# Kernel optimization log

Measured on AMD Instinct MI355X. Metric: run time of the kernel, lower is better.

The kernel has to match this reference:

```python
import jax, jax.numpy as jnp
import numpy as np

NLAYERS = 4
HEADS = 4
HEAD_DIM = 64
C = HEADS * HEAD_DIM  # 256
MAX_LEN = 1024


def setup_inputs() -> dict:
    key = jax.random.key(0)
    k1, k2, k3 = jax.random.split(key, 3)
    B, S = 16, 1024
    x = jax.random.normal(k1, (B, C, 1, S), dtype=jnp.float32)
    # length is only used via its static shape[0]; values are irrelevant
    length = jnp.zeros((MAX_LEN,), dtype=jnp.int32)
    # per-layer 1x1 conv weights, std=0.1 as in the torch init (squeeze the 1x1 spatial dims)
    w = jax.random.normal(k2, (NLAYERS, C, C), dtype=jnp.float32) * 0.1
    # persistent kv buffer
    kv = jax.random.normal(k3, (NLAYERS, HEADS, MAX_LEN, HEAD_DIM), dtype=jnp.float32) * 0.1
    return {"x": x, "length": length, "w": w, "kv": kv}


def reference(x, length, w, kv):
    B, _, _, S = x.shape
    L = length.shape[0]  # static slice length into kv buffer
    scale = 1.0 / jnp.sqrt(jnp.asarray(HEAD_DIM, dtype=x.dtype))
    for i in range(NLAYERS):
        # 1x1 conv == channel projection: (B,C,1,S) -> (B,C,1,S)
        x = jnp.einsum('oc,bchs->bohs', w[i], x)
        # view (B,4,64,S) then permute -> query (B,H,S,D)
        q = x.reshape(B, HEADS, HEAD_DIM, S).transpose(0, 1, 3, 2)
        kvi = kv[i, :, :L]  # (H, L, D); broadcasts over batch like the (1,H,L,D) torch slice
        # scaled dot-product attention with k == v == kvi
        scores = jnp.einsum('bhsd,hld->bhsl', q, kvi) * scale
        attn = jax.nn.softmax(scores, axis=-1)
        o = jnp.einsum('bhsl,hld->bhsd', attn, kvi)  # (B,H,S,D)
        # permute back and merge heads -> (B,256,1,S)
        x = o.transpose(0, 1, 3, 2).reshape(B, C, 1, S)
    return x
```

## Files before the change

kernel.cpp:

```cpp
#include <hip/hip_runtime.h>

#define NL   4
#define NH   4
#define HD   64
#define CD   256
#define SQL  1024
#define BB   16

typedef _Float16 half8 __attribute__((ext_vector_type(8)));
typedef _Float16 half4 __attribute__((ext_vector_type(4)));
typedef _Float16 half2v __attribute__((ext_vector_type(2)));
typedef float    f32x4 __attribute__((ext_vector_type(4)));
typedef unsigned short u16x8 __attribute__((ext_vector_type(8)));

static __device__ __forceinline__ float bf2f(unsigned short u) {
    union { unsigned int i; float f; } v; v.i = ((unsigned int)u) << 16; return v.f;
}
static __device__ __forceinline__ unsigned short f2bf(float f) {
    union { float f; unsigned int i; } v; v.f = f;
    unsigned int u = v.i;
    return (unsigned short)((u + 0x7fffu + ((u >> 16) & 1u)) >> 16);
}

static __device__ __forceinline__ int detect_flag(const void* win) {
    const unsigned int* w = (const unsigned int*)win;
    int cnt = 0;
#pragma unroll 1
    for (int i = 0; i < 64; i++) {
        unsigned int lo = w[i] & 0xFFFFu;
        int e = (int)((lo >> 7) & 0xFF);
        cnt += (e >= 96 && e <= 144) ? 1 : 0;
    }
    return cnt >= 48 ? 1 : 0;
}

__global__ __launch_bounds__(256) void prep_all(const void* __restrict__ xin,
                                                const void* __restrict__ win,
                                                const void* __restrict__ kvin,
                                                _Float16* __restrict__ x16,
                                                _Float16* __restrict__ w16,
                                                _Float16* __restrict__ kaF,
                                                _Float16* __restrict__ vtF) {
    __shared__ __align__(16) _Float16 tile[64][72];
    const int bi = blockIdx.x;
    const int t = threadIdx.x;
    const int isbf = detect_flag(win);

    if (bi < 1024) {
        const int st = bi & 15, ct = (bi >> 4) & 3, b = bi >> 6;
        const int r = t >> 2, seg = t & 3;
        const size_t base = ((size_t)(b * CD + ct * 64 + r)) * SQL + st * 64 + seg * 16;
        float v[16];
        if (isbf) {
            const unsigned short* src = (const unsigned short*)xin + base;
            u16x8 u0 = *(const u16x8*)(src);
            u16x8 u1 = *(const u16x8*)(src + 8);
#pragma unroll
            for (int j = 0; j < 8; j++) { v[j] = bf2f(u0[j]); v[8 + j] = bf2f(u1[j]); }
        } else {
            const float* src = (const float*)xin + base;
#pragma unroll
            for (int c = 0; c < 4; c++) {
                f32x4 a = *(const f32x4*)(src + c * 4);
#pragma unroll
                for (int j = 0; j < 4; j++) v[c * 4 + j] = a[j];
            }
        }
#pragma unroll
        for (int j = 0; j < 16; j++) tile[r][seg * 16 + j] = (_Float16)v[j];
        __syncthreads();
        half8 o0, o1;
#pragma unroll
        for (int j = 0; j < 8; j++) { o0[j] = tile[seg * 16 + j][r]; o1[j] = tile[seg * 16 + 8 + j][r]; }
        _Float16* dt = x16 + ((size_t)(b * SQL + st * 64 + r)) * CD + ct * 64 + seg * 16;
        *(half8*)(dt) = o0;
        *(half8*)(dt + 8) = o1;
    } else if (bi < 1280) {
        const int j2 = bi - 1024;
        const int lt = j2 & 15, ih = j2 >> 4;
        const int r = t >> 2, seg = t & 3;
        const size_t base = ((size_t)(ih * SQL + lt * 64 + r)) * HD + seg * 16;
        float v[16];
        if (isbf) {
            const unsigned short* src = (const unsigned short*)kvin + base;
            u16x8 u0 = *(const u16x8*)(src);
            u16x8 u1 = *(const u16x8*)(src + 8);
#pragma unroll
            for (int j = 0; j < 8; j++) { v[j] = bf2f(u0[j]); v[8 + j] = bf2f(u1[j]); }
        } else {
            const float* src = (const float*)kvin + base;
#pragma unroll
            for (int c = 0; c < 4; c++) {
                f32x4 a = *(const f32x4*)(src + c * 4);
#pragma unroll
                for (int j = 0; j < 4; j++) v[c * 4 + j] = a[j];
            }
        }
#pragma unroll
        for (int j = 0; j < 16; j++) tile[r][seg * 16 + j] = (_Float16)v[j];
        __syncthreads();
        const int l = t & 63, l16 = l & 15, q = l >> 4;
        _Float16* kaB = kaF + ((size_t)ih << 16);
        _Float16* vtB = vtF + ((size_t)ih << 16);
#pragma unroll
        for (int it = 0; it < 2; it++) {
            const int c = (t >> 6) + it * 4;
            const int kd = c >> 1, msp = c & 1;
            half8 ok, ov;
#pragma unroll
            for (int j = 0; j < 4; j++) {
                ok[j]     = tile[msp * 32 + l16][kd * 16 + q * 4 + j];
                ok[4 + j] = tile[msp * 32 + 16 + l16][kd * 16 + q * 4 + j];
                ov[j]     = tile[kd * 16 + q * 4 + j][msp * 32 + l16];
                ov[4 + j] = tile[kd * 16 + q * 4 + j][msp * 32 + 16 + l16];
            }
            *(half8*)(kaB + ((lt * 8 + c) << 9) + l * 8) = ok;
            *(half8*)(vtB + ((lt * 8 + c) << 9) + l * 8) = ov;
        }
    } else {
        const int i = (bi - 1280) * 256 + t;
        const size_t base = (size_t)i * 8;
        half8 h;
        if (isbf) {
            u16x8 u = *(const u16x8*)((const unsigned short*)win + base);
#pragma unroll
            for (int j = 0; j < 8; j++) h[j] = (_Float16)bf2f(u[j]);
        } else {
            const float* p = (const float*)win + base;
            f32x4 a0 = *(const f32x4*)(p);
            f32x4 a1 = *(const f32x4*)(p + 4);
#pragma unroll
            for (int j = 0; j < 4; j++) { h[j] = (_Float16)a0[j]; h[4 + j] = (_Float16)a1[j]; }
        }
        *(half8*)(w16 + base) = h;
    }
}

__global__ __launch_bounds__(256, 2) void layer_fused(const _Float16* __restrict__ xg,
                                                      _Float16* __restrict__ xout,
                                                      const _Float16* __restrict__ w16,
                                                      const _Float16* __restrict__ kaF,
                                                      const _Float16* __restrict__ vtF,
                                                      const void* __restrict__ win,
                                                      void* __restrict__ outp,
                                                      int L) {
    const int sb = blockIdx.x;
    const int h  = blockIdx.y;
    const int b  = blockIdx.z;
    const int t  = threadIdx.x;
    const int wv = t >> 6, lane = t & 63, l16 = lane & 15, quad = lane >> 4;
    const int s0 = sb * 128 + wv * 32;

    f32x4 gacc[4][2];
#pragma unroll
    for (int md = 0; md < 4; md++)
#pragma unroll
        for (int nt = 0; nt < 2; nt++)
#pragma unroll
            for (int r = 0; r < 4; r++) gacc[md][nt][r] = 0.0f;
    const _Float16* wb = w16 + ((size_t)L << 16) + ((size_t)(h * 64) << 8);
#pragma unroll
    for (int kk = 0; kk < 8; kk++) {
        half8 bx[2];
#pragma unroll
        for (int nt = 0; nt < 2; nt++)
            bx[nt] = *(const half8*)(xg + ((size_t)((b << 10) + s0 + nt * 16 + l16) << 8) +
                                     kk * 32 + quad * 8);
#pragma unroll
        for (int md = 0; md < 4; md++) {
            half8 aw = *(const half8*)(wb + ((size_t)(md * 16 + l16) << 8) + kk * 32 + quad * 8);
            gacc[md][0] = __builtin_amdgcn_mfma_f32_16x16x32_f16(aw, bx[0], gacc[md][0], 0, 0, 0);
            gacc[md][1] = __builtin_amdgcn_mfma_f32_16x16x32_f16(aw, bx[1], gacc[md][1], 0, 0, 0);
        }
    }
    half4 qh[4][2];
#pragma unroll
    for (int md = 0; md < 4; md++)
#pragma unroll
        for (int nt = 0; nt < 2; nt++)
#pragma unroll
            for (int r = 0; r < 4; r++)
                qh[md][nt][r] = (_Float16)(gacc[md][nt][r] * 0.180336880111120f);

    half4 ones4;
#pragma unroll
    for (int r = 0; r < 4; r++) ones4[r] = (_Float16)1.0f;

    const _Float16* kaB = kaF + ((size_t)(L * NH + h) << 16);
    const _Float16* vtB = vtF + ((size_t)(L * NH + h) << 16);

    f32x4 oacc[4][2];
    f32x4 osum[2];
#pragma unroll
    for (int md = 0; md < 4; md++)
#pragma unroll
        for (int nt = 0; nt < 2; nt++)
#pragma unroll
            for (int r = 0; r < 4; r++) oacc[md][nt][r] = 0.0f;
#pragma unroll
    for (int nt = 0; nt < 2; nt++)
#pragma unroll
        for (int r = 0; r < 4; r++) osum[nt][r] = 0.0f;

    half8 kab[2][8];
    half8 vab[8];
    f32x4 sttC[4][2];

    auto loadK = [&](int lt, int buf) {
#pragma unroll
        for (int c = 0; c < 8; c++)
            kab[buf][c] = *(const half8*)(kaB + (((lt * 8 + c) << 9) + lane * 8));
    };
    auto loadV = [&](int lt) {
#pragma unroll
        for (int c = 0; c < 8; c++)
            vab[c] = *(const half8*)(vtB + (((lt * 8 + c) << 9) + lane * 8));
    };
    auto doQK = [&](int buf) {
#pragma unroll
        for (int ms = 0; ms < 4; ms++)
#pragma unroll
            for (int nt = 0; nt < 2; nt++)
#pragma unroll
                for (int r = 0; r < 4; r++) sttC[ms][nt][r] = 0.0f;
#pragma unroll
        for (int kd = 0; kd < 4; kd++)
#pragma unroll
            for (int msp = 0; msp < 2; msp++) {
                half8 kk8 = kab[buf][kd * 2 + msp];
                half4 lo = __builtin_shufflevector(kk8, kk8, 0, 1, 2, 3);
                half4 hi = __builtin_shufflevector(kk8, kk8, 4, 5, 6, 7);
#pragma unroll
                for (int nt = 0; nt < 2; nt++) {
                    sttC[msp * 2][nt] = __builtin_amdgcn_mfma_f32_16x16x16f16(
                        lo, qh[kd][nt], sttC[msp * 2][nt], 0, 0, 0);
                    sttC[msp * 2 + 1][nt] = __builtin_amdgcn_mfma_f32_16x16x16f16(
                        hi, qh[kd][nt], sttC[msp * 2 + 1][nt], 0, 0, 0);
                }
            }
    };

    loadK(0, 0);
    loadK(1, 1);
    doQK(0);

#pragma unroll 2
    for (int lt = 0; lt < 16; lt++) {
        const int cb = lt & 1, nb = cb ^ 1;
        if (lt < 14) loadK(lt + 2, cb);
        loadV(lt);

        half4 pb[4][2];
#pragma unroll
        for (int ms = 0; ms < 4; ms++)
#pragma unroll
            for (int nt = 0; nt < 2; nt++) {
                float e0 = __builtin_amdgcn_exp2f(sttC[ms][nt][0]);
                float e1 = __builtin_amdgcn_exp2f(sttC[ms][nt][1]);
                float e2 = __builtin_amdgcn_exp2f(sttC[ms][nt][2]);
                float e3 = __builtin_amdgcn_exp2f(sttC[ms][nt][3]);
                half2v p01 = __builtin_bit_cast(half2v, __builtin_amdgcn_cvt_pkrtz(e0, e1));
                half2v p23 = __builtin_bit_cast(half2v, __builtin_amdgcn_cvt_pkrtz(e2, e3));
                pb[ms][nt] = __builtin_shufflevector(p01, p23, 0, 1, 2, 3);
            }

        if (lt < 15) doQK(nb);

#pragma unroll
        for (int ks = 0; ks < 4; ks++) {
#pragma unroll
            for (int nt = 0; nt < 2; nt++)
                osum[nt] = __builtin_amdgcn_mfma_f32_16x16x16f16(
                    ones4, pb[ks][nt], osum[nt], 0, 0, 0);
#pragma unroll
            for (int mdp = 0; mdp < 2; mdp++) {
                half8 vv8 = vab[ks * 2 + mdp];
                half4 lo = __builtin_shufflevector(vv8, vv8, 0, 1, 2, 3);
                half4 hi = __builtin_shufflevector(vv8, vv8, 4, 5, 6, 7);
#pragma unroll
                for (int nt = 0; nt < 2; nt++) {
                    oacc[mdp * 2][nt] = __builtin_amdgcn_mfma_f32_16x16x16f16(
                        lo, pb[ks][nt], oacc[mdp * 2][nt], 0, 0, 0);
                    oacc[mdp * 2 + 1][nt] = __builtin_amdgcn_mfma_f32_16x16x16f16(
                        hi, pb[ks][nt], oacc[mdp * 2 + 1][nt], 0, 0, 0);
                }
            }
        }
    }

    float inv[2];
#pragma unroll
    for (int nt = 0; nt < 2; nt++) inv[nt] = 1.0f / osum[nt][0];

    if (L < NL - 1) {
#pragma unroll
        for (int md = 0; md < 4; md++)
#pragma unroll
            for (int nt = 0; nt < 2; nt++) {
                const int s = s0 + nt * 16 + l16;
                half4 hv;
#pragma unroll
                for (int r = 0; r < 4; r++) hv[r] = (_Float16)(oacc[md][nt][r] * inv[nt]);
                *(half4*)(xout + (((size_t)((b << 10) + s)) << 8) + (h << 6) + md * 16 + quad * 4) = hv;
            }
    } else if (detect_flag(win)) {
#pragma unroll
        for (int md = 0; md < 4; md++)
#pragma unroll
            for (int nt = 0; nt < 2; nt++) {
                const int s = s0 + nt * 16 + l16;
#pragma unroll
                for (int r = 0; r < 4; r++) {
                    const int c = (h << 6) + md * 16 + quad * 4 + r;
                    ((unsigned short*)outp)[(((size_t)(b * CD + c)) << 10) + s] =
                        f2bf(oacc[md][nt][r] * inv[nt]);
                }
            }
    } else {
#pragma unroll
        for (int md = 0; md < 4; md++)
#pragma unroll
            for (int nt = 0; nt < 2; nt++) {
                const int s = s0 + nt * 16 + l16;
#pragma unroll
                for (int r = 0; r < 4; r++) {
                    const int c = (h << 6) + md * 16 + quad * 4 + r;
                    ((float*)outp)[(((size_t)(b * CD + c)) << 10) + s] =
                        oacc[md][nt][r] * inv[nt];
                }
            }
    }
}

extern "C" void kernel_launch(void* const* d_in, const int* in_sizes, int n_in,
                              void* d_out, int out_size, void* d_ws, size_t ws_size,
                              hipStream_t stream) {
    const void* xin = d_in[0];
    const void* win = d_in[2];
    const void* kvin = d_in[3];

    char* ws = (char*)d_ws;
    const size_t MB = 1u << 20;
    _Float16* xa  = (_Float16*)(ws);
    _Float16* xb  = (_Float16*)(ws + 8 * MB);
    _Float16* w16 = (_Float16*)(ws + 16 * MB);
    _Float16* kaF = (_Float16*)(ws + 17 * MB);
    _Float16* vtF = (_Float16*)(ws + 19 * MB);

    prep_all<<<dim3(1024 + 256 + 128), 256, 0, stream>>>(xin, win, kvin, xa, w16, kaF, vtF);

    _Float16* cur = xa;
    _Float16* nxt = xb;
    for (int i = 0; i < NL; i++) {
        layer_fused<<<dim3(SQL / 128, NH, BB), 256, 0, stream>>>(cur, nxt, w16, kaF, vtF,
                                                                 win, d_out, i);
        _Float16* tmp = cur; cur = nxt; nxt = tmp;
    }
}
```

Measured before the change: 249.0 us.

## Split KV range across wave pairs and combine partial attention in shared memory

```diff
diff --git a/kernel.cpp b/kernel.cpp
--- a/kernel.cpp
+++ b/kernel.cpp
@@ -136,7 +136,7 @@
     }
 }
 
-__global__ __launch_bounds__(256, 2) void layer_fused(const _Float16* __restrict__ xg,
+__global__ __launch_bounds__(256, 4) void layer_fused(const _Float16* __restrict__ xg,
                                                       _Float16* __restrict__ xout,
                                                       const _Float16* __restrict__ w16,
                                                       const _Float16* __restrict__ kaF,
@@ -144,12 +144,15 @@
                                                       const void* __restrict__ win,
                                                       void* __restrict__ outp,
                                                       int L) {
+    __shared__ __align__(16) f32x4 comb[2][9][64];
     const int sb = blockIdx.x;
     const int h  = blockIdx.y;
     const int b  = blockIdx.z;
     const int t  = threadIdx.x;
     const int wv = t >> 6, lane = t & 63, l16 = lane & 15, quad = lane >> 4;
-    const int s0 = sb * 128 + wv * 32;
+    const int pair = wv & 1;
+    const int lhalf = wv >> 1;
+    const int s0 = sb * 64 + pair * 32;
 
     f32x4 gacc[4][2];
 #pragma unroll
@@ -188,6 +191,7 @@
 
     const _Float16* kaB = kaF + ((size_t)(L * NH + h) << 16);
     const _Float16* vtB = vtF + ((size_t)(L * NH + h) << 16);
+    const int lt0 = lhalf * 8;
 
     f32x4 oacc[4][2];
     f32x4 osum[2];
@@ -240,15 +244,15 @@
             }
     };
 
-    loadK(0, 0);
-    loadK(1, 1);
+    loadK(lt0, 0);
+    loadK(lt0 + 1, 1);
     doQK(0);
 
 #pragma unroll 2
-    for (int lt = 0; lt < 16; lt++) {
-        const int cb = lt & 1, nb = cb ^ 1;
-        if (lt < 14) loadK(lt + 2, cb);
-        loadV(lt);
+    for (int i = 0; i < 8; i++) {
+        const int cb = i & 1, nb = cb ^ 1;
+        if (i < 6) loadK(lt0 + i + 2, cb);
+        loadV(lt0 + i);
 
         half4 pb[4][2];
 #pragma unroll
@@ -264,7 +268,7 @@
                 pb[ms][nt] = __builtin_shufflevector(p01, p23, 0, 1, 2, 3);
             }
 
-        if (lt < 15) doQK(nb);
+        if (i < 7) doQK(nb);
 
 #pragma unroll
         for (int ks = 0; ks < 4; ks++) {
@@ -288,47 +292,69 @@
         }
     }
 
-    float inv[2];
-#pragma unroll
-    for (int nt = 0; nt < 2; nt++) inv[nt] = 1.0f / osum[nt][0];
-
-    if (L < NL - 1) {
+    if (lhalf == 1) {
 #pragma unroll
         for (int md = 0; md < 4; md++)
 #pragma unroll
+            for (int nt = 0; nt < 2; nt++)
+                comb[pair][md * 2 + nt][lane] = oacc[md][nt];
+        f32x4 ls;
+        ls[0] = osum[0][0]; ls[1] = osum[1][0]; ls[2] = 0.0f; ls[3] = 0.0f;
+        comb[pair][8][lane] = ls;
+    }
+    __syncthreads();
+    if (lhalf == 0) {
+#pragma unroll
+        for (int md = 0; md < 4; md++)
+#pragma unroll
             for (int nt = 0; nt < 2; nt++) {
-                const int s = s0 + nt * 16 + l16;
-                half4 hv;
-#pragma unroll
-                for (int r = 0; r < 4; r++) hv[r] = (_Float16)(oacc[md][nt][r] * inv[nt]);
-                *(half4*)(xout + (((size_t)((b << 10) + s)) << 8) + (h << 6) + md * 16 + quad * 4) = hv;
-            }
-    } else if (detect_flag(win)) {
-#pragma unroll
-        for (int md = 0; md < 4; md++)
-#pragma unroll
-            for (int nt = 0; nt < 2; nt++) {
-                const int s = s0 + nt * 16 + l16;
-#pragma unroll
-                for (int r = 0; r < 4; r++) {
-                    const int c = (h << 6) + md * 16 + quad * 4 + r;
-                    ((unsigned short*)outp)[(((size_t)(b * CD + c)) << 10) + s] =
-                        f2bf(oacc[md][nt][r] * inv[nt]);
-                }
-            }
-    } else {
-#pragma unroll
-        for (int md = 0; md < 4; md++)
-#pragma unroll
-            for (int nt = 0; nt < 2; nt++) {
-                const int s = s0 + nt * 16 + l16;
-#pragma unroll
-                for (int r = 0; r < 4; r++) {
-                    const int c = (h << 6) + md * 16 + quad * 4 + r;
-                    ((float*)outp)[(((size_t)(b * CD + c)) << 10) + s] =
-                        oacc[md][nt][r] * inv[nt];
-                }
-            }
+                f32x4 o2 = comb[pair][md * 2 + nt][lane];
+#pragma unroll
+                for (int r = 0; r < 4; r++) oacc[md][nt][r] += o2[r];
+            }
+        f32x4 ls = comb[pair][8][lane];
+        float inv[2];
+        inv[0] = 1.0f / (osum[0][0] + ls[0]);
+        inv[1] = 1.0f / (osum[1][0] + ls[1]);
+
+        if (L < NL - 1) {
+#pragma unroll
+            for (int md = 0; md < 4; md++)
+#pragma unroll
+                for (int nt = 0; nt < 2; nt++) {
+                    const int s = s0 + nt * 16 + l16;
+                    half4 hv;
+#pragma unroll
+                    for (int r = 0; r < 4; r++) hv[r] = (_Float16)(oacc[md][nt][r] * inv[nt]);
+                    *(half4*)(xout + (((size_t)((b << 10) + s)) << 8) + (h << 6) + md * 16 + quad * 4) = hv;
+                }
+        } else if (detect_flag(win)) {
+#pragma unroll
+            for (int md = 0; md < 4; md++)
+#pragma unroll
+                for (int nt = 0; nt < 2; nt++) {
+                    const int s = s0 + nt * 16 + l16;
+#pragma unroll
+                    for (int r = 0; r < 4; r++) {
+                        const int c = (h << 6) + md * 16 + quad * 4 + r;
+                        ((unsigned short*)outp)[(((size_t)(b * CD + c)) << 10) + s] =
+                            f2bf(oacc[md][nt][r] * inv[nt]);
+                    }
+                }
+        } else {
+#pragma unroll
+            for (int md = 0; md < 4; md++)
+#pragma unroll
+                for (int nt = 0; nt < 2; nt++) {
+                    const int s = s0 + nt * 16 + l16;
+#pragma unroll
+                    for (int r = 0; r < 4; r++) {
+                        const int c = (h << 6) + md * 16 + quad * 4 + r;
+                        ((float*)outp)[(((size_t)(b * CD + c)) << 10) + s] =
+                            oacc[md][nt][r] * inv[nt];
+                    }
+                }
+        }
     }
 }
 
@@ -352,8 +378,8 @@
     _Float16* cur = xa;
     _Float16* nxt = xb;
     for (int i = 0; i < NL; i++) {
-        layer_fused<<<dim3(SQL / 128, NH, BB), 256, 0, stream>>>(cur, nxt, w16, kaF, vtF,
-                                                                 win, d_out, i);
+        layer_fused<<<dim3(SQL / 64, NH, BB), 256, 0, stream>>>(cur, nxt, w16, kaF, vtF,
+                                                                win, d_out, i);
         _Float16* tmp = cur; cur = nxt; nxt = tmp;
     }
 }
```

After: 743.2 us. 2.98x slower.
